# Performance work log

Hardware: AMD Instinct MI355X
Metric: run time of the kernel (lower is better)

The kernel has to match this reference:

```python
import math
import jax, jax.numpy as jnp
import numpy as np

BATCH = 65536
SIZE = 1024


def _even_odd_mult(p, x):
    """(1-p)*x + p*[evens..., odds...] for x of shape (B, n)."""
    B, n = x.shape
    sep = x.reshape(B, n // 2, 2).transpose(0, 2, 1).reshape(B, n)
    return (1 - p) * x + p * sep


def _reverse_mult(p1, p2, x):
    """Probabilistically reverse first half (p1) and second half (p2)."""
    B, n = x.shape
    h = n // 2
    first = x[:, :h]
    second = x[:, h:]
    first = (1 - p1) * first + p1 * first[:, ::-1]
    second = (1 - p2) * second + p2 * second[:, ::-1]
    return jnp.concatenate([first, second], axis=-1)


def setup_inputs() -> dict:
    key = jax.random.key(0)
    k1, k2 = jax.random.split(key)
    x = jax.random.normal(k1, (BATCH, SIZE), dtype=jnp.float32)
    m = int(math.log2(SIZE))
    logits = jax.random.normal(k2, (m - 1, 3), dtype=jnp.float32)
    return {"x": x, "logits": logits}


def reference(x, logits):
    size = x.shape[-1]
    m = int(math.log2(size))
    # factor i has size sizes[i]; increasing_size=True -> [4, 8, ..., size]
    sizes = [size >> i for i in range(m - 1)][::-1]
    out = x
    # forward iterates factors[::-1]: largest block size first
    for i in range(m - 2, -1, -1):
        n = sizes[i]
        prob = jax.nn.sigmoid(logits[i])
        y = out.reshape(-1, n)
        y = _even_odd_mult(prob[0], y)
        y = _reverse_mult(prob[1], prob[2], y)
        out = y.reshape(out.shape)
    return out
```

## Files before the change

kernel.cpp:

```cpp
#include <hip/hip_runtime.h>
#include <math.h>

#define TPB 256
#define ROWS 8

__device__ __forceinline__ unsigned swz(unsigned A) {
    return A ^ ((((A >> 8) ^ (A >> 11)) & 7u) << 4);
}

__device__ __forceinline__ float4 ldsrd(const char* ldsb, unsigned A) {
    return *(const float4*)(ldsb + A);
}

template<int N>
__device__ __forceinline__ void lds_stage(char* ldsb, unsigned rb, unsigned tt,
                                          float p, float p1, float p2) {
    constexpr unsigned H = N / 2;
    constexpr int L2 = (N == 1024) ? 5 : (N == 512) ? 4 : (N == 256) ? 3
                     : (N == 128) ? 2 : 1;
    const unsigned b  = tt >> L2;
    const unsigned s  = tt & ((N / 32) - 1);
    const unsigned u0 = s * 8u;
    const unsigned bc = b * (unsigned)N;

    const unsigned Aj0  = swz(rb + 4u * (bc + u0));
    const unsigned Aj1  = swz(rb + 4u * (bc + H + u0));
    const unsigned Ajm0 = swz(rb + 4u * (bc + H - 8 - u0));
    const unsigned Ajm1 = swz(rb + 4u * (bc + N - 8 - u0));
    const unsigned Ae   = swz(rb + 4u * (bc + 2 * u0));
    const unsigned Aem  = swz(rb + 4u * (bc + 2 * H - 16 - 2 * u0));

    float j0[8], j1[8], jm0[8], jm1[8], e[16], em[16];
    *(float4*)&j0[0]  = ldsrd(ldsb, Aj0);        *(float4*)&j0[4]  = ldsrd(ldsb, Aj0 ^ 16u);
    *(float4*)&j1[0]  = ldsrd(ldsb, Aj1);        *(float4*)&j1[4]  = ldsrd(ldsb, Aj1 ^ 16u);
    *(float4*)&jm0[0] = ldsrd(ldsb, Ajm0);       *(float4*)&jm0[4] = ldsrd(ldsb, Ajm0 ^ 16u);
    *(float4*)&jm1[0] = ldsrd(ldsb, Ajm1);       *(float4*)&jm1[4] = ldsrd(ldsb, Ajm1 ^ 16u);
    *(float4*)&e[0]   = ldsrd(ldsb, Ae);         *(float4*)&e[4]   = ldsrd(ldsb, Ae ^ 16u);
    *(float4*)&e[8]   = ldsrd(ldsb, Ae ^ 32u);   *(float4*)&e[12]  = ldsrd(ldsb, Ae ^ 48u);
    *(float4*)&em[0]  = ldsrd(ldsb, Aem);        *(float4*)&em[4]  = ldsrd(ldsb, Aem ^ 16u);
    *(float4*)&em[8]  = ldsrd(ldsb, Aem ^ 32u);  *(float4*)&em[12] = ldsrd(ldsb, Aem ^ 48u);

    #pragma unroll
    for (int du = 0; du < 8; ++du) {
        {
            float yj = j0[du], yjm = jm0[7 - du];
            float yej = e[2 * du], yejm = em[14 - 2 * du];
            float a0 = fmaf(p, yej - yj, yj);
            float a1 = fmaf(p, yejm - yjm, yjm);
            float d  = a1 - a0;
            j0[du]      = fmaf(p1, d, a0);
            jm0[7 - du] = fmaf(p1, -d, a1);
        }
        {
            float zj = j1[du], zjm = jm1[7 - du];
            float zej = e[2 * du + 1], zejm = em[15 - 2 * du];
            float a0 = fmaf(p, zej - zj, zj);
            float a1 = fmaf(p, zejm - zjm, zjm);
            float d  = a1 - a0;
            j1[du]      = fmaf(p2, d, a0);
            jm1[7 - du] = fmaf(p2, -d, a1);
        }
    }
    __syncthreads();
    *(float4*)(ldsb + Aj0)          = *(const float4*)&j0[0];
    *(float4*)(ldsb + (Aj0 ^ 16u))  = *(const float4*)&j0[4];
    *(float4*)(ldsb + Aj1)          = *(const float4*)&j1[0];
    *(float4*)(ldsb + (Aj1 ^ 16u))  = *(const float4*)&j1[4];
    *(float4*)(ldsb + Ajm0)         = *(const float4*)&jm0[0];
    *(float4*)(ldsb + (Ajm0 ^ 16u)) = *(const float4*)&jm0[4];
    *(float4*)(ldsb + Ajm1)         = *(const float4*)&jm1[0];
    *(float4*)(ldsb + (Ajm1 ^ 16u)) = *(const float4*)&jm1[4];
    __syncthreads();
}

template<int N>
__device__ __forceinline__ void reg_stage(float* arr, float p, float p1, float p2) {
    constexpr int H = N / 2;
    float tmp[32];
    #pragma unroll
    for (int bb = 0; bb < 32; bb += N) {
        #pragma unroll
        for (int u = 0; u < N / 4; ++u) {
            {
                int j = bb + u, jm = bb + H - 1 - u;
                int ej = bb + 2 * u, ejm = bb + 2 * H - 2 - 2 * u;
                float a0 = fmaf(p, arr[ej]  - arr[j],  arr[j]);
                float a1 = fmaf(p, arr[ejm] - arr[jm], arr[jm]);
                tmp[j]  = fmaf(p1, a1 - a0, a0);
                tmp[jm] = fmaf(p1, a0 - a1, a1);
            }
            {
                int j = bb + H + u, jm = bb + 2 * H - 1 - u;
                int ej = bb + 2 * u + 1, ejm = bb + 2 * H - 1 - 2 * u;
                float a0 = fmaf(p, arr[ej]  - arr[j],  arr[j]);
                float a1 = fmaf(p, arr[ejm] - arr[jm], arr[jm]);
                tmp[j]  = fmaf(p2, a1 - a0, a0);
                tmp[jm] = fmaf(p2, a0 - a1, a1);
            }
        }
    }
    #pragma unroll
    for (int v = 0; v < 32; ++v) arr[v] = tmp[v];
}

__global__ void bpp_prep(const float* __restrict__ logits, float* __restrict__ sp) {
    int i = threadIdx.x;
    if (i < 27) sp[i] = 1.0f / (1.0f + expf(-logits[i]));
}

template<bool USE_WS>
__global__ __launch_bounds__(TPB) void bpp_main(const float* __restrict__ x,
                                                float* __restrict__ out,
                                                const float* __restrict__ spws,
                                                const float* __restrict__ logits) {
    __shared__ float lds[ROWS * 1024];
    char* ldsb = (char*)lds;
    const unsigned t = threadIdx.x;
    const size_t gbase = (size_t)blockIdx.x * (ROWS * 1024);

    float prl[27];
    if constexpr (!USE_WS) {
        #pragma unroll
        for (int i = 0; i < 27; ++i) prl[i] = 1.0f / (1.0f + expf(-logits[i]));
    }
    #define PV(i) (USE_WS ? spws[(i)] : prl[(i)])

    const float4* __restrict__ gin = (const float4*)(x + gbase);
    #pragma unroll
    for (int k = 0; k < 8; ++k) {
        float4 v = gin[k * TPB + t];
        unsigned A = (unsigned)k * 4096u + t * 16u;
        *(float4*)(ldsb + swz(A)) = v;
    }
    __syncthreads();

    const unsigned row = t >> 5, tt = t & 31u;
    const unsigned rb = row * 4096u;

    lds_stage<1024>(ldsb, rb, tt, PV(24), PV(25), PV(26));
    lds_stage< 512>(ldsb, rb, tt, PV(21), PV(22), PV(23));
    lds_stage< 256>(ldsb, rb, tt, PV(18), PV(19), PV(20));
    lds_stage< 128>(ldsb, rb, tt, PV(15), PV(16), PV(17));
    lds_stage<  64>(ldsb, rb, tt, PV(12), PV(13), PV(14));

    {
        unsigned A = rb + tt * 128u;
        unsigned SB = swz(A);
        float arr[32];
        #pragma unroll
        for (int k = 0; k < 8; ++k)
            *(float4*)&arr[4 * k] = *(const float4*)(ldsb + (SB ^ (16u * k)));
        reg_stage<32>(arr, PV(9), PV(10), PV(11));
        reg_stage<16>(arr, PV(6), PV(7),  PV(8));
        reg_stage< 8>(arr, PV(3), PV(4),  PV(5));
        reg_stage< 4>(arr, PV(0), PV(1),  PV(2));
        #pragma unroll
        for (int k = 0; k < 8; ++k)
            *(float4*)(ldsb + (SB ^ (16u * k))) = *(const float4*)&arr[4 * k];
    }
    __syncthreads();

    float4* __restrict__ gout = (float4*)(out + gbase);
    #pragma unroll
    for (int k = 0; k < 8; ++k) {
        unsigned A = (unsigned)k * 4096u + t * 16u;
        gout[k * TPB + t] = *(const float4*)(ldsb + swz(A));
    }
    #undef PV
}

extern "C" void kernel_launch(void* const* d_in, const int* in_sizes, int n_in,
                              void* d_out, int out_size, void* d_ws, size_t ws_size,
                              hipStream_t stream) {
    const float* x      = (const float*)d_in[0];
    const float* logits = (const float*)d_in[1];
    float* out = (float*)d_out;
    int rows = in_sizes[0] / 1024;
    int grid = rows / ROWS;
    if (ws_size >= 27 * sizeof(float)) {
        float* sp = (float*)d_ws;
        bpp_prep<<<dim3(1), dim3(32), 0, stream>>>(logits, sp);
        bpp_main<true><<<dim3(grid), dim3(TPB), 0, stream>>>(x, out, sp, logits);
    } else {
        bpp_main<false><<<dim3(grid), dim3(TPB), 0, stream>>>(x, out, nullptr, logits);
    }
}
```

Baseline: 137.7 us.

## Fuse first butterfly stage into global load and last LDS stage into register store

The N=1024 stage now reads its operands straight from global memory into registers and writes only its results to LDS, which removes the initial global-to-LDS copy and one LDS round trip. The N=64 stage now runs from registers: each thread pulls its own 32-element half plus the partner half and then continues directly into the register stages. Results are written directly to global memory, dropping the final LDS write, barrier and readback. In exchange, global loads and stores are less coalesced (per-thread 32-byte and mirrored strided accesses, 128-byte stores per thread) and register pressure rises.

```diff
diff --git a/kernel.cpp b/kernel.cpp
--- a/kernel.cpp
+++ b/kernel.cpp
@@ -2,7 +2,6 @@
 #include <math.h>
 
 #define TPB 256
-#define ROWS 8
 
 __device__ __forceinline__ unsigned swz(unsigned A) {
     return A ^ ((((A >> 8) ^ (A >> 11)) & 7u) << 4);
@@ -16,8 +15,7 @@
 __device__ __forceinline__ void lds_stage(char* ldsb, unsigned rb, unsigned tt,
                                           float p, float p1, float p2) {
     constexpr unsigned H = N / 2;
-    constexpr int L2 = (N == 1024) ? 5 : (N == 512) ? 4 : (N == 256) ? 3
-                     : (N == 128) ? 2 : 1;
+    constexpr int L2 = (N == 512) ? 4 : (N == 256) ? 3 : 2;
     const unsigned b  = tt >> L2;
     const unsigned s  = tt & ((N / 32) - 1);
     const unsigned u0 = s * 8u;
@@ -113,10 +111,10 @@
                                                 float* __restrict__ out,
                                                 const float* __restrict__ spws,
                                                 const float* __restrict__ logits) {
-    __shared__ float lds[ROWS * 1024];
+    __shared__ float lds[8 * 1024];
     char* ldsb = (char*)lds;
     const unsigned t = threadIdx.x;
-    const size_t gbase = (size_t)blockIdx.x * (ROWS * 1024);
+    const size_t gbase = (size_t)blockIdx.x * (8 * 1024);
 
     float prl[27];
     if constexpr (!USE_WS) {
@@ -125,46 +123,111 @@
     }
     #define PV(i) (USE_WS ? spws[(i)] : prl[(i)])
 
-    const float4* __restrict__ gin = (const float4*)(x + gbase);
-    #pragma unroll
-    for (int k = 0; k < 8; ++k) {
-        float4 v = gin[k * TPB + t];
-        unsigned A = (unsigned)k * 4096u + t * 16u;
-        *(float4*)(ldsb + swz(A)) = v;
+    {
+        const unsigned row = t >> 5, tt = t & 31u;
+        const unsigned rb = row * 4096u;
+        const float* __restrict__ gr = x + gbase + row * 1024u;
+        const float p = PV(24), p1 = PV(25), p2 = PV(26);
+
+        float j0[8], j1[8], jm0[8], jm1[8], e[16], em[16];
+        #define LD4(dst, off) *(float4*)&(dst) = *(const float4*)(gr + (off))
+        LD4(j0[0],  8u * tt);            LD4(j0[4],  8u * tt + 4u);
+        LD4(j1[0],  512u + 8u * tt);     LD4(j1[4],  516u + 8u * tt);
+        LD4(jm0[0], 504u - 8u * tt);     LD4(jm0[4], 508u - 8u * tt);
+        LD4(jm1[0], 1016u - 8u * tt);    LD4(jm1[4], 1020u - 8u * tt);
+        LD4(e[0],   16u * tt);           LD4(e[4],   16u * tt + 4u);
+        LD4(e[8],   16u * tt + 8u);      LD4(e[12],  16u * tt + 12u);
+        LD4(em[0],  1008u - 16u * tt);   LD4(em[4],  1012u - 16u * tt);
+        LD4(em[8],  1016u - 16u * tt);   LD4(em[12], 1020u - 16u * tt);
+        #undef LD4
+
+        #pragma unroll
+        for (int du = 0; du < 8; ++du) {
+            {
+                float yj = j0[du], yjm = jm0[7 - du];
+                float yej = e[2 * du], yejm = em[14 - 2 * du];
+                float a0 = fmaf(p, yej - yj, yj);
+                float a1 = fmaf(p, yejm - yjm, yjm);
+                float d  = a1 - a0;
+                j0[du]      = fmaf(p1, d, a0);
+                jm0[7 - du] = fmaf(p1, -d, a1);
+            }
+            {
+                float zj = j1[du], zjm = jm1[7 - du];
+                float zej = e[2 * du + 1], zejm = em[15 - 2 * du];
+                float a0 = fmaf(p, zej - zj, zj);
+                float a1 = fmaf(p, zejm - zjm, zjm);
+                float d  = a1 - a0;
+                j1[du]      = fmaf(p2, d, a0);
+                jm1[7 - du] = fmaf(p2, -d, a1);
+            }
+        }
+        const unsigned Aj0  = swz(rb + 32u * tt);
+        const unsigned Aj1  = swz(rb + 2048u + 32u * tt);
+        const unsigned Ajm0 = swz(rb + 2016u - 32u * tt);
+        const unsigned Ajm1 = swz(rb + 4064u - 32u * tt);
+        *(float4*)(ldsb + Aj0)          = *(const float4*)&j0[0];
+        *(float4*)(ldsb + (Aj0 ^ 16u))  = *(const float4*)&j0[4];
+        *(float4*)(ldsb + Aj1)          = *(const float4*)&j1[0];
+        *(float4*)(ldsb + (Aj1 ^ 16u))  = *(const float4*)&j1[4];
+        *(float4*)(ldsb + Ajm0)         = *(const float4*)&jm0[0];
+        *(float4*)(ldsb + (Ajm0 ^ 16u)) = *(const float4*)&jm0[4];
+        *(float4*)(ldsb + Ajm1)         = *(const float4*)&jm1[0];
+        *(float4*)(ldsb + (Ajm1 ^ 16u)) = *(const float4*)&jm1[4];
     }
     __syncthreads();
 
-    const unsigned row = t >> 5, tt = t & 31u;
-    const unsigned rb = row * 4096u;
-
-    lds_stage<1024>(ldsb, rb, tt, PV(24), PV(25), PV(26));
-    lds_stage< 512>(ldsb, rb, tt, PV(21), PV(22), PV(23));
-    lds_stage< 256>(ldsb, rb, tt, PV(18), PV(19), PV(20));
-    lds_stage< 128>(ldsb, rb, tt, PV(15), PV(16), PV(17));
-    lds_stage<  64>(ldsb, rb, tt, PV(12), PV(13), PV(14));
-
     {
-        unsigned A = rb + tt * 128u;
-        unsigned SB = swz(A);
-        float arr[32];
+        const unsigned row = t >> 5, tt = t & 31u;
+        const unsigned rb = row * 4096u;
+        lds_stage<512>(ldsb, rb, tt, PV(21), PV(22), PV(23));
+        lds_stage<256>(ldsb, rb, tt, PV(18), PV(19), PV(20));
+        lds_stage<128>(ldsb, rb, tt, PV(15), PV(16), PV(17));
+    }
+
+    {
+        const unsigned r5 = t & 7u, b5 = (t >> 3) & 15u, h5 = t >> 7;
+        const unsigned base = r5 * 4096u + b5 * 256u + h5 * 128u;
+        const unsigned So = swz(base);
+        const unsigned St = So ^ 128u;
+        float own[32], oth[32];
+        #pragma unroll
+        for (int k = 0; k < 8; ++k) {
+            *(float4*)&own[4 * k] = ldsrd(ldsb, So ^ (16u * k));
+            *(float4*)&oth[4 * k] = ldsrd(ldsb, St ^ (16u * k));
+        }
+        const float p = PV(12), p1 = PV(13), p2 = PV(14);
+        float o[32];
+        if (h5 == 0) {
+            #pragma unroll
+            for (int u = 0; u < 16; ++u) {
+                float yj = own[u], yjm = own[31 - u];
+                float a0 = fmaf(p, own[2 * u] - yj, yj);
+                float a1 = fmaf(p, oth[30 - 2 * u] - yjm, yjm);
+                float d  = a1 - a0;
+                o[u]      = fmaf(p1, d, a0);
+                o[31 - u] = fmaf(p1, -d, a1);
+            }
+        } else {
+            #pragma unroll
+            for (int u = 0; u < 16; ++u) {
+                float yj = own[u], yjm = own[31 - u];
+                float a0 = fmaf(p, oth[2 * u + 1] - yj, yj);
+                float a1 = fmaf(p, own[31 - 2 * u] - yjm, yjm);
+                float d  = a1 - a0;
+                o[u]      = fmaf(p2, d, a0);
+                o[31 - u] = fmaf(p2, -d, a1);
+            }
+        }
+        reg_stage<32>(o, PV(9), PV(10), PV(11));
+        reg_stage<16>(o, PV(6), PV(7),  PV(8));
+        reg_stage< 8>(o, PV(3), PV(4),  PV(5));
+        reg_stage< 4>(o, PV(0), PV(1),  PV(2));
+
+        float* __restrict__ go = out + gbase + r5 * 1024u + b5 * 64u + h5 * 32u;
         #pragma unroll
         for (int k = 0; k < 8; ++k)
-            *(float4*)&arr[4 * k] = *(const float4*)(ldsb + (SB ^ (16u * k)));
-        reg_stage<32>(arr, PV(9), PV(10), PV(11));
-        reg_stage<16>(arr, PV(6), PV(7),  PV(8));
-        reg_stage< 8>(arr, PV(3), PV(4),  PV(5));
-        reg_stage< 4>(arr, PV(0), PV(1),  PV(2));
-        #pragma unroll
-        for (int k = 0; k < 8; ++k)
-            *(float4*)(ldsb + (SB ^ (16u * k))) = *(const float4*)&arr[4 * k];
-    }
-    __syncthreads();
-
-    float4* __restrict__ gout = (float4*)(out + gbase);
-    #pragma unroll
-    for (int k = 0; k < 8; ++k) {
-        unsigned A = (unsigned)k * 4096u + t * 16u;
-        gout[k * TPB + t] = *(const float4*)(ldsb + swz(A));
+            *(float4*)(go + 4 * k) = *(const float4*)&o[4 * k];
     }
     #undef PV
 }
@@ -176,7 +239,7 @@
     const float* logits = (const float*)d_in[1];
     float* out = (float*)d_out;
     int rows = in_sizes[0] / 1024;
-    int grid = rows / ROWS;
+    int grid = rows / 8;
     if (ws_size >= 27 * sizeof(float)) {
         float* sp = (float*)d_ws;
         bpp_prep<<<dim3(1), dim3(32), 0, stream>>>(logits, sp);
```

Measured after the change: 154.1 us. 1.12x slower.
